# Performance work log

Measured on AMD Instinct MI355X. Metric: run time of the kernel, lower is better.

The kernel has to match this reference:

```python
import jax, jax.numpy as jnp
import numpy as np

N, E, G = 100000, 1600000, 2000
D_IN, D_H, D_MLP, D_OUT = 768, 128, 32, 2


def setup_inputs() -> dict:
    key = jax.random.key(0)
    ks = jax.random.split(key, 12)
    x = jax.random.normal(ks[0], (N, D_IN), dtype=jnp.float32)
    edge_index = jax.random.randint(ks[1], (2, E), 0, N, dtype=jnp.int64)
    edge_attr = jax.random.uniform(ks[2], (E, 1), dtype=jnp.float32)
    batch = jnp.sort(jax.random.randint(ks[3], (N,), 0, G, dtype=jnp.int64))
    s1 = 1.0 / np.sqrt(D_IN)
    s2 = 1.0 / np.sqrt(D_H)
    s3 = 1.0 / np.sqrt(D_MLP)
    return {
        "x": x, "edge_index": edge_index, "edge_attr": edge_attr,
        "batch": batch, "num_graphs": G,
        "W1i": jax.random.normal(ks[4], (D_IN, D_H), dtype=jnp.float32) * s1,
        "W1r": jax.random.normal(ks[5], (D_IN, D_H), dtype=jnp.float32) * s1,
        "b1": jnp.zeros((D_H,), dtype=jnp.float32),
        "W2i": jax.random.normal(ks[6], (D_H, D_H), dtype=jnp.float32) * s2,
        "W2r": jax.random.normal(ks[7], (D_H, D_H), dtype=jnp.float32) * s2,
        "b2": jnp.zeros((D_H,), dtype=jnp.float32),
        "Wl1": jax.random.normal(ks[8], (D_H, D_MLP), dtype=jnp.float32) * s2,
        "bl1": jnp.zeros((D_MLP,), dtype=jnp.float32),
        "Wl2": jax.random.normal(ks[9], (D_MLP, D_OUT), dtype=jnp.float32) * s3,
        "bl2": jnp.zeros((D_OUT,), dtype=jnp.float32),
    }


def _arma_conv(x, row, col, ew, Wi, Wr, b, n_nodes):
    # gcn_norm without self-loops: D^{-1/2} A D^{-1/2}
    deg = jax.ops.segment_sum(ew, col, num_segments=n_nodes)
    dinv = jnp.where(deg > 0, jax.lax.rsqrt(jnp.where(deg > 0, deg, 1.0)), 0.0)
    norm = dinv[row] * ew * dinv[col]
    h = x @ Wi                                   # [N, F_out]
    msg = h[row] * norm[:, None]                 # gather + scale  [E, F_out]
    agg = jax.ops.segment_sum(msg, col, num_segments=n_nodes)
    return jax.nn.relu(agg + x @ Wr + b)         # ARMA: K=1, T=1, act=ReLU


def reference(x, edge_index, edge_attr, batch, num_graphs,
              W1i, W1r, b1, W2i, W2r, b2, Wl1, bl1, Wl2, bl2):
    row, col = edge_index[0], edge_index[1]
    ew = edge_attr.reshape(-1)
    n = x.shape[0]
    h = jax.nn.elu(_arma_conv(x, row, col, ew, W1i, W1r, b1, n))
    node_x = _arma_conv(h, row, col, ew, W2i, W2r, b2, n)
    # global mean pool over graphs
    sums = jax.ops.segment_sum(node_x, batch, num_segments=num_graphs)
    cnt = jax.ops.segment_sum(jnp.ones((n,), node_x.dtype), batch, num_segments=num_graphs)
    graph_x = sums / jnp.maximum(cnt, 1.0)[:, None]
    pred = jax.nn.elu(graph_x @ Wl1 + bl1) @ Wl2 + bl2
    return pred
```

## Files before the change

kernel.cpp:

```cpp
#include <hip/hip_runtime.h>
#include <hip/hip_bf16.h>
#include <math.h>

typedef __attribute__((ext_vector_type(8))) short short8;
typedef __attribute__((ext_vector_type(4))) float f32x4;
typedef __attribute__((ext_vector_type(2))) float f32x2;
typedef __attribute__((address_space(1))) const void gvoid;
typedef __attribute__((address_space(3))) void lvoid;

#define NC 8

__device__ __forceinline__ unsigned short f2bf(float f) {
    unsigned int u = __builtin_bit_cast(unsigned int, f);
    return (unsigned short)((u + 0x7fffu + ((u >> 16) & 1u)) >> 16);
}
__device__ __forceinline__ float b2f(short s) {
    return __builtin_bit_cast(float, ((unsigned int)(unsigned short)s) << 16);
}
__device__ __forceinline__ unsigned int cvtpk(float lo, float hi) {
    unsigned int r;
    asm("v_cvt_pk_bf16_f32 %0, %1, %2" : "=v"(r) : "v"(lo), "v"(hi));
    return r;
}
__device__ __forceinline__ unsigned int pk8_lo(float a, float b, unsigned int old) {
    return (unsigned int)__builtin_amdgcn_cvt_pk_fp8_f32(a, b, (int)old, false);
}
__device__ __forceinline__ unsigned int pk8_hi(float a, float b, unsigned int old) {
    return (unsigned int)__builtin_amdgcn_cvt_pk_fp8_f32(a, b, (int)old, true);
}
__device__ __forceinline__ f32x2 up8_lo(unsigned int v) {
    return __builtin_amdgcn_cvt_pk_f32_fp8((int)v, false);
}
__device__ __forceinline__ f32x2 up8_hi(unsigned int v) {
    return __builtin_amdgcn_cvt_pk_f32_fp8((int)v, true);
}

__global__ __launch_bounds__(256) void deg_hist_kernel(
    const int* __restrict__ ei, const float* __restrict__ ea,
    unsigned long long* __restrict__ packed, int* __restrict__ rank, int N, int E)
{
    int e = blockIdx.x * 256 + threadIdx.x;
    if (e >= E) return;
    const int copy = blockIdx.x & (NC - 1);
    int c = ei[(size_t)E + e];
    unsigned long long fx = (unsigned long long)(ea[e] * 1048576.0f + 0.5f);
    unsigned long long old = atomicAdd(&packed[(size_t)copy * N + c], (1ULL << 42) | fx);
    rank[e] = (int)(old >> 42);
}

__global__ __launch_bounds__(256) void scan1p_kernel(
    const unsigned long long* __restrict__ packed, int* __restrict__ out,
    int* __restrict__ blksum, int n)
{
    __shared__ int part[256];
    const int t = threadIdx.x;
    const int base = blockIdx.x * 1024 + t * 4;
    int v[4];
#pragma unroll
    for (int q = 0; q < 4; ++q) {
        int s = 0;
        if (base + q < n) {
#pragma unroll
            for (int p = 0; p < NC; ++p)
                s += (int)(packed[(size_t)p * n + base + q] >> 42);
        }
        v[q] = s;
    }
    const int s = v[0] + v[1] + v[2] + v[3];
    part[t] = s;
    __syncthreads();
    for (int off = 1; off < 256; off <<= 1) {
        int x = (t >= off) ? part[t - off] : 0;
        __syncthreads();
        part[t] += x;
        __syncthreads();
    }
    if (t == 255) blksum[blockIdx.x] = part[255];
    int run = part[t] - s;
#pragma unroll
    for (int q = 0; q < 4; ++q) {
        if (base + q < n) out[base + q] = run;
        run += v[q];
    }
}

__global__ __launch_bounds__(256) void scan1_kernel(
    const int* __restrict__ in, int* __restrict__ out, int* __restrict__ blksum, int n)
{
    __shared__ int part[256];
    const int t = threadIdx.x;
    const int base = blockIdx.x * 1024 + t * 4;
    int v[4];
#pragma unroll
    for (int q = 0; q < 4; ++q) v[q] = (base + q < n) ? in[base + q] : 0;
    const int s = v[0] + v[1] + v[2] + v[3];
    part[t] = s;
    __syncthreads();
    for (int off = 1; off < 256; off <<= 1) {
        int x = (t >= off) ? part[t - off] : 0;
        __syncthreads();
        part[t] += x;
        __syncthreads();
    }
    if (t == 255) blksum[blockIdx.x] = part[255];
    int run = part[t] - s;
#pragma unroll
    for (int q = 0; q < 4; ++q) {
        if (base + q < n) out[base + q] = run;
        run += v[q];
    }
}

__global__ __launch_bounds__(256) void scan3_kernel(
    int* __restrict__ rowptr, const int* __restrict__ blkoff,
    int* __restrict__ wpb, const unsigned long long* __restrict__ packed,
    float* __restrict__ dinv, int n, int Etot)
{
    int i = blockIdx.x * 256 + threadIdx.x;
    if (i == 0) rowptr[n] = Etot;
    if (i >= n) return;
    int base = rowptr[i] + blkoff[i >> 10];
    rowptr[i] = base;
    unsigned long long degfx = 0;
    int acc = base;
#pragma unroll
    for (int p = 0; p < NC; ++p) {
        unsigned long long v = packed[(size_t)p * n + i];
        wpb[(size_t)p * n + i] = acc;
        acc += (int)(v >> 42);
        degfx += v & ((1ULL << 42) - 1);
    }
    dinv[i] = (degfx > 0) ? rsqrtf((float)degfx * 9.5367431640625e-7f) : 0.f;
}

__global__ __launch_bounds__(256) void place_kernel(
    const int* __restrict__ ei, const float* __restrict__ ea,
    const float* __restrict__ dinv, const int* __restrict__ wpb,
    const int* __restrict__ rank, int2* __restrict__ csr, int N, int E)
{
    int e = blockIdx.x * 256 + threadIdx.x;
    if (e >= E) return;
    const int copy = blockIdx.x & (NC - 1);
    int r = ei[e];
    int c = ei[(size_t)E + e];
    float nm = dinv[r] * ea[e] * dinv[c];
    int pos = wpb[(size_t)copy * N + c] + rank[e];
    int2 rec;
    rec.x = r;
    rec.y = __builtin_bit_cast(int, nm);
    csr[pos] = rec;
}

__global__ __launch_bounds__(256) void conv_weights(
    const float* __restrict__ W1i, const float* __restrict__ W1r,
    const float* __restrict__ W2i, const float* __restrict__ W2r,
    unsigned short* __restrict__ W1t, unsigned short* __restrict__ W2t)
{
    int id = blockIdx.x * 256 + threadIdx.x;
    if (id < 256 * 768) {
        int n = id / 768, j = id % 768;
        int k = (j & ~63) | ((((j >> 3) & 7) ^ (n & 7)) << 3) | (j & 7);
        float v = (n < 128) ? W1i[k * 128 + n] : W1r[k * 128 + (n - 128)];
        W1t[id] = f2bf(v);
    } else {
        int id2 = id - 256 * 768;
        if (id2 < 128 * 256) {
            int n = id2 >> 8, j = id2 & 255;
            int k = (j & ~63) | ((((j >> 3) & 7) ^ (n & 7)) << 3) | (j & 7);
            float v = (k < 128) ? W2i[k * 128 + n] : W2r[(k - 128) * 128 + n];
            W2t[id2] = f2bf(v);
        }
    }
}

__global__ __launch_bounds__(512) void gemm_mfma_dual(
    const float* __restrict__ A, const unsigned short* __restrict__ Wt,
    const float* __restrict__ bias, unsigned char* __restrict__ outP8,
    unsigned short* __restrict__ outR, int M, int K)
{
    __shared__ __align__(16) unsigned char As[2][64 * 128];
    __shared__ __align__(16) unsigned char Bs[2][256 * 128];

    const int t = threadIdx.x;
    const int m0 = blockIdx.x * 64;
    const int lane = t & 63;
    const int wid = t >> 6;
    const int wm = wid >> 2;
    const int wn = wid & 3;
    const int lr = lane & 15;
    const int lk = (lane >> 4) * 8;

    f32x4 acc[2][4] = {};

    const int sr = t >> 3;
    const int sk = (t & 7) * 8;
    const int aRow = m0 + sr;
    const bool aOk = (aRow < M);
    const float* aSrc = A + (size_t)(aOk ? aRow : 0) * K + sk;
    const int aDst = sr * 128 + ((sk * 2) ^ ((sr & 7) << 4));
    const unsigned short* bSrc = Wt + (size_t)(lane >> 3) * K + (lane & 7) * 8;

#pragma unroll
    for (int i = 0; i < 4; ++i) {
        const int chunk = i * 8 + wid;
        __builtin_amdgcn_global_load_lds(
            (gvoid*)(bSrc + (size_t)chunk * 8 * K),
            (lvoid*)(&Bs[0][chunk * 1024]), 16, 0, 0);
    }
    {
        float4 f0 = {}, f1 = {};
        if (aOk) { f0 = *(const float4*)(aSrc); f1 = *(const float4*)(aSrc + 4); }
        uint4 uv = {cvtpk(f0.x, f0.y), cvtpk(f0.z, f0.w),
                    cvtpk(f1.x, f1.y), cvtpk(f1.z, f1.w)};
        *(uint4*)(&As[0][aDst]) = uv;
    }

    for (int k0 = 0; k0 < K; k0 += 64) {
        const int cur = (k0 >> 6) & 1;
        const int nxt = cur ^ 1;
        const bool hasNext = (k0 + 64 < K);
        __syncthreads();

        float4 g0 = {}, g1 = {};
        if (hasNext) {
#pragma unroll
            for (int i = 0; i < 4; ++i) {
                const int chunk = i * 8 + wid;
                __builtin_amdgcn_global_load_lds(
                    (gvoid*)(bSrc + (size_t)chunk * 8 * K + k0 + 64),
                    (lvoid*)(&Bs[nxt][chunk * 1024]), 16, 0, 0);
            }
            if (aOk) {
                g0 = *(const float4*)(aSrc + k0 + 64);
                g1 = *(const float4*)(aSrc + k0 + 64 + 4);
            }
        }

#pragma unroll
        for (int ks = 0; ks < 2; ++ks) {
            short8 a[2], b[4];
#pragma unroll
            for (int mf = 0; mf < 2; ++mf) {
                const int r = wm * 32 + mf * 16 + lr;
                a[mf] = *(const short8*)(&As[cur][r * 128 + (((ks * 32 + lk) * 2) ^ ((r & 7) << 4))]);
            }
#pragma unroll
            for (int nf = 0; nf < 4; ++nf) {
                const int n = wn * 64 + nf * 16 + lr;
                b[nf] = *(const short8*)(&Bs[cur][n * 128 + (((ks * 32 + lk) * 2) ^ ((n & 7) << 4))]);
            }
#pragma unroll
            for (int mf = 0; mf < 2; ++mf)
#pragma unroll
                for (int nf = 0; nf < 4; ++nf)
                    acc[mf][nf] = __builtin_amdgcn_mfma_f32_16x16x32_bf16(
                        a[mf], b[nf], acc[mf][nf], 0, 0, 0);
        }

        if (hasNext) {
            uint4 uv = {cvtpk(g0.x, g0.y), cvtpk(g0.z, g0.w),
                        cvtpk(g1.x, g1.y), cvtpk(g1.z, g1.w)};
            *(uint4*)(&As[nxt][aDst]) = uv;
        }
    }

#pragma unroll
    for (int mf = 0; mf < 2; ++mf) {
#pragma unroll
        for (int nf = 0; nf < 4; ++nf) {
            const int n = wn * 64 + nf * 16 + lr;
            const f32x4 v = acc[mf][nf];
            const int mb = m0 + wm * 32 + mf * 16 + (lane >> 4) * 4;
            if (n < 128) {
                const unsigned int u01 = pk8_lo(v[0], v[1], 0u);
                const unsigned int u23 = pk8_lo(v[2], v[3], 0u);
                if (mb + 0 < M) outP8[(size_t)(mb + 0) * 128 + n] = (unsigned char)(u01);
                if (mb + 1 < M) outP8[(size_t)(mb + 1) * 128 + n] = (unsigned char)(u01 >> 8);
                if (mb + 2 < M) outP8[(size_t)(mb + 2) * 128 + n] = (unsigned char)(u23);
                if (mb + 3 < M) outP8[(size_t)(mb + 3) * 128 + n] = (unsigned char)(u23 >> 8);
            } else {
                const int nl = n - 128;
                const float badd = bias[nl];
#pragma unroll
                for (int j = 0; j < 4; ++j) {
                    if (mb + j < M) outR[(size_t)(mb + j) * 128 + nl] = f2bf(v[j] + badd);
                }
            }
        }
    }
}

__global__ __launch_bounds__(512) void gemm_mfma_single(
    const unsigned short* __restrict__ Aa,
    const unsigned short* __restrict__ Ah,
    const unsigned short* __restrict__ Wt,
    const float* __restrict__ bias,
    unsigned short* __restrict__ outX, int M)
{
    __shared__ __align__(16) unsigned char As[128 * 128];
    __shared__ __align__(16) unsigned char Bs[128 * 128];

    const int t = threadIdx.x;
    const int m0 = blockIdx.x * 128;
    const int lane = t & 63;
    const int wid = t >> 6;
    const int wm = wid >> 1;
    const int wn = wid & 1;
    const int lr = lane & 15;
    const int lk = (lane >> 4) * 8;

    f32x4 acc[2][4] = {};

    const int sr = t >> 2;
    const int sk = (t & 3) * 16;
    const int aRow = m0 + sr;
    const bool aOk = (aRow < M);
    const int rowSafe = aOk ? aRow : 0;
    const int sw = (sr & 7) << 4;
    const unsigned short* bSrc = Wt + (size_t)(lane >> 3) * 256 + (lane & 7) * 8;

    for (int k0 = 0; k0 < 256; k0 += 64) {
#pragma unroll
        for (int i = 0; i < 2; ++i) {
            const int chunk = i * 8 + wid;
            __builtin_amdgcn_global_load_lds(
                (gvoid*)(bSrc + (size_t)chunk * 8 * 256 + k0),
                (lvoid*)(Bs + chunk * 1024), 16, 0, 0);
        }
        const unsigned short* src =
            (k0 < 128 ? Aa : Ah) + (size_t)rowSafe * 128 + (k0 & 127) + sk;
        const short8 v0 = *(const short8*)(src);
        const short8 v1 = *(const short8*)(src + 8);
        *(short8*)(As + sr * 128 + ((sk * 2) ^ sw)) = v0;
        *(short8*)(As + sr * 128 + ((sk * 2 + 16) ^ sw)) = v1;
        __syncthreads();
#pragma unroll
        for (int ks = 0; ks < 2; ++ks) {
            short8 a[2], b[4];
#pragma unroll
            for (int mf = 0; mf < 2; ++mf) {
                const int r = wm * 32 + mf * 16 + lr;
                a[mf] = *(const short8*)(As + r * 128 + (((ks * 32 + lk) * 2) ^ ((r & 7) << 4)));
            }
#pragma unroll
            for (int nf = 0; nf < 4; ++nf) {
                const int n = wn * 64 + nf * 16 + lr;
                b[nf] = *(const short8*)(Bs + n * 128 + (((ks * 32 + lk) * 2) ^ ((n & 7) << 4)));
            }
#pragma unroll
            for (int mf = 0; mf < 2; ++mf)
#pragma unroll
                for (int nf = 0; nf < 4; ++nf)
                    acc[mf][nf] = __builtin_amdgcn_mfma_f32_16x16x32_bf16(
                        a[mf], b[nf], acc[mf][nf], 0, 0, 0);
        }
        __syncthreads();
    }

#pragma unroll
    for (int mf = 0; mf < 2; ++mf) {
#pragma unroll
        for (int nf = 0; nf < 4; ++nf) {
            const int n = wn * 64 + nf * 16 + lr;
            const float bb = bias[n];
            const f32x4 v = acc[mf][nf];
#pragma unroll
            for (int j = 0; j < 4; ++j) {
                const int m = m0 + wm * 32 + mf * 16 + (lane >> 4) * 4 + j;
                if (m < M) outX[(size_t)m * 128 + n] = f2bf(fmaxf(v[j] + bb, 0.f));
            }
        }
    }
}

__global__ __launch_bounds__(256) void agg_bias_relu(
    const unsigned char* __restrict__ P8, const unsigned short* __restrict__ Rbf,
    const int* __restrict__ rowptr, const int2* __restrict__ csr,
    unsigned short* __restrict__ hout, unsigned char* __restrict__ h8out, int N)
{
    const int i = blockIdx.x * 16 + (threadIdx.x >> 4);
    const int l = threadIdx.x & 15;
    if (i >= N) return;
    const int beg = rowptr[i];
    const int end = rowptr[i + 1];
    const int c = l * 8;

    float acc0[8] = {}, acc1[8] = {}, acc2[8] = {}, acc3[8] = {};
    int j = beg;
    for (; j + 3 < end; j += 4) {
        const int2 e0 = csr[j],     e1 = csr[j + 1];
        const int2 e2 = csr[j + 2], e3 = csr[j + 3];
        const uint2 u0 = *(const uint2*)(P8 + (size_t)e0.x * 128 + c);
        const uint2 u1 = *(const uint2*)(P8 + (size_t)e1.x * 128 + c);
        const uint2 u2 = *(const uint2*)(P8 + (size_t)e2.x * 128 + c);
        const uint2 u3 = *(const uint2*)(P8 + (size_t)e3.x * 128 + c);
        const float n0 = __builtin_bit_cast(float, e0.y);
        const float n1 = __builtin_bit_cast(float, e1.y);
        const float n2 = __builtin_bit_cast(float, e2.y);
        const float n3 = __builtin_bit_cast(float, e3.y);
        {
            const f32x2 p0 = up8_lo(u0.x), p1 = up8_hi(u0.x);
            const f32x2 p2 = up8_lo(u0.y), p3 = up8_hi(u0.y);
            acc0[0] = fmaf(p0.x, n0, acc0[0]); acc0[1] = fmaf(p0.y, n0, acc0[1]);
            acc0[2] = fmaf(p1.x, n0, acc0[2]); acc0[3] = fmaf(p1.y, n0, acc0[3]);
            acc0[4] = fmaf(p2.x, n0, acc0[4]); acc0[5] = fmaf(p2.y, n0, acc0[5]);
            acc0[6] = fmaf(p3.x, n0, acc0[6]); acc0[7] = fmaf(p3.y, n0, acc0[7]);
        }
        {
            const f32x2 p0 = up8_lo(u1.x), p1 = up8_hi(u1.x);
            const f32x2 p2 = up8_lo(u1.y), p3 = up8_hi(u1.y);
            acc1[0] = fmaf(p0.x, n1, acc1[0]); acc1[1] = fmaf(p0.y, n1, acc1[1]);
            acc1[2] = fmaf(p1.x, n1, acc1[2]); acc1[3] = fmaf(p1.y, n1, acc1[3]);
            acc1[4] = fmaf(p2.x, n1, acc1[4]); acc1[5] = fmaf(p2.y, n1, acc1[5]);
            acc1[6] = fmaf(p3.x, n1, acc1[6]); acc1[7] = fmaf(p3.y, n1, acc1[7]);
        }
        {
            const f32x2 p0 = up8_lo(u2.x), p1 = up8_hi(u2.x);
            const f32x2 p2 = up8_lo(u2.y), p3 = up8_hi(u2.y);
            acc2[0] = fmaf(p0.x, n2, acc2[0]); acc2[1] = fmaf(p0.y, n2, acc2[1]);
            acc2[2] = fmaf(p1.x, n2, acc2[2]); acc2[3] = fmaf(p1.y, n2, acc2[3]);
            acc2[4] = fmaf(p2.x, n2, acc2[4]); acc2[5] = fmaf(p2.y, n2, acc2[5]);
            acc2[6] = fmaf(p3.x, n2, acc2[6]); acc2[7] = fmaf(p3.y, n2, acc2[7]);
        }
        {
            const f32x2 p0 = up8_lo(u3.x), p1 = up8_hi(u3.x);
            const f32x2 p2 = up8_lo(u3.y), p3 = up8_hi(u3.y);
            acc3[0] = fmaf(p0.x, n3, acc3[0]); acc3[1] = fmaf(p0.y, n3, acc3[1]);
            acc3[2] = fmaf(p1.x, n3, acc3[2]); acc3[3] = fmaf(p1.y, n3, acc3[3]);
            acc3[4] = fmaf(p2.x, n3, acc3[4]); acc3[5] = fmaf(p2.y, n3, acc3[5]);
            acc3[6] = fmaf(p3.x, n3, acc3[6]); acc3[7] = fmaf(p3.y, n3, acc3[7]);
        }
    }
    for (; j < end; ++j) {
        const int2 e0 = csr[j];
        const uint2 u0 = *(const uint2*)(P8 + (size_t)e0.x * 128 + c);
        const float n0 = __builtin_bit_cast(float, e0.y);
        const f32x2 p0 = up8_lo(u0.x), p1 = up8_hi(u0.x);
        const f32x2 p2 = up8_lo(u0.y), p3 = up8_hi(u0.y);
        acc0[0] = fmaf(p0.x, n0, acc0[0]); acc0[1] = fmaf(p0.y, n0, acc0[1]);
        acc0[2] = fmaf(p1.x, n0, acc0[2]); acc0[3] = fmaf(p1.y, n0, acc0[3]);
        acc0[4] = fmaf(p2.x, n0, acc0[4]); acc0[5] = fmaf(p2.y, n0, acc0[5]);
        acc0[6] = fmaf(p3.x, n0, acc0[6]); acc0[7] = fmaf(p3.y, n0, acc0[7]);
    }
    const short8 rv = *(const short8*)(Rbf + (size_t)i * 128 + c);
    float s[8];
    short8 ov;
#pragma unroll
    for (int q = 0; q < 8; ++q) {
        s[q] = fmaxf((acc0[q] + acc1[q]) + (acc2[q] + acc3[q]) + b2f(rv[q]), 0.f);
        ov[q] = (short)f2bf(s[q]);
    }
    *(short8*)(hout + (size_t)i * 128 + c) = ov;
    unsigned int w0 = 0, w1 = 0;
    w0 = pk8_lo(s[0], s[1], w0); w0 = pk8_hi(s[2], s[3], w0);
    w1 = pk8_lo(s[4], s[5], w1); w1 = pk8_hi(s[6], s[7], w1);
    uint2 wv = {w0, w1};
    *(uint2*)(h8out + (size_t)i * 128 + c) = wv;
}

__global__ __launch_bounds__(256) void agg_plain(
    const unsigned char* __restrict__ H8,
    const int* __restrict__ rowptr, const int2* __restrict__ csr,
    unsigned short* __restrict__ ahout, int N)
{
    const int i = blockIdx.x * 16 + (threadIdx.x >> 4);
    const int l = threadIdx.x & 15;
    if (i >= N) return;
    const int beg = rowptr[i];
    const int end = rowptr[i + 1];
    const int c = l * 8;

    float acc0[8] = {}, acc1[8] = {}, acc2[8] = {}, acc3[8] = {};
    int j = beg;
    for (; j + 3 < end; j += 4) {
        const int2 e0 = csr[j],     e1 = csr[j + 1];
        const int2 e2 = csr[j + 2], e3 = csr[j + 3];
        const uint2 u0 = *(const uint2*)(H8 + (size_t)e0.x * 128 + c);
        const uint2 u1 = *(const uint2*)(H8 + (size_t)e1.x * 128 + c);
        const uint2 u2 = *(const uint2*)(H8 + (size_t)e2.x * 128 + c);
        const uint2 u3 = *(const uint2*)(H8 + (size_t)e3.x * 128 + c);
        const float n0 = __builtin_bit_cast(float, e0.y);
        const float n1 = __builtin_bit_cast(float, e1.y);
        const float n2 = __builtin_bit_cast(float, e2.y);
        const float n3 = __builtin_bit_cast(float, e3.y);
        {
            const f32x2 p0 = up8_lo(u0.x), p1 = up8_hi(u0.x);
            const f32x2 p2 = up8_lo(u0.y), p3 = up8_hi(u0.y);
            acc0[0] = fmaf(p0.x, n0, acc0[0]); acc0[1] = fmaf(p0.y, n0, acc0[1]);
            acc0[2] = fmaf(p1.x, n0, acc0[2]); acc0[3] = fmaf(p1.y, n0, acc0[3]);
            acc0[4] = fmaf(p2.x, n0, acc0[4]); acc0[5] = fmaf(p2.y, n0, acc0[5]);
            acc0[6] = fmaf(p3.x, n0, acc0[6]); acc0[7] = fmaf(p3.y, n0, acc0[7]);
        }
        {
            const f32x2 p0 = up8_lo(u1.x), p1 = up8_hi(u1.x);
            const f32x2 p2 = up8_lo(u1.y), p3 = up8_hi(u1.y);
            acc1[0] = fmaf(p0.x, n1, acc1[0]); acc1[1] = fmaf(p0.y, n1, acc1[1]);
            acc1[2] = fmaf(p1.x, n1, acc1[2]); acc1[3] = fmaf(p1.y, n1, acc1[3]);
            acc1[4] = fmaf(p2.x, n1, acc1[4]); acc1[5] = fmaf(p2.y, n1, acc1[5]);
            acc1[6] = fmaf(p3.x, n1, acc1[6]); acc1[7] = fmaf(p3.y, n1, acc1[7]);
        }
        {
            const f32x2 p0 = up8_lo(u2.x), p1 = up8_hi(u2.x);
            const f32x2 p2 = up8_lo(u2.y), p3 = up8_hi(u2.y);
            acc2[0] = fmaf(p0.x, n2, acc2[0]); acc2[1] = fmaf(p0.y, n2, acc2[1]);
            acc2[2] = fmaf(p1.x, n2, acc2[2]); acc2[3] = fmaf(p1.y, n2, acc2[3]);
            acc2[4] = fmaf(p2.x, n2, acc2[4]); acc2[5] = fmaf(p2.y, n2, acc2[5]);
            acc2[6] = fmaf(p3.x, n2, acc2[6]); acc2[7] = fmaf(p3.y, n2, acc2[7]);
        }
        {
            const f32x2 p0 = up8_lo(u3.x), p1 = up8_hi(u3.x);
            const f32x2 p2 = up8_lo(u3.y), p3 = up8_hi(u3.y);
            acc3[0] = fmaf(p0.x, n3, acc3[0]); acc3[1] = fmaf(p0.y, n3, acc3[1]);
            acc3[2] = fmaf(p1.x, n3, acc3[2]); acc3[3] = fmaf(p1.y, n3, acc3[3]);
            acc3[4] = fmaf(p2.x, n3, acc3[4]); acc3[5] = fmaf(p2.y, n3, acc3[5]);
            acc3[6] = fmaf(p3.x, n3, acc3[6]); acc3[7] = fmaf(p3.y, n3, acc3[7]);
        }
    }
    for (; j < end; ++j) {
        const int2 e0 = csr[j];
        const uint2 u0 = *(const uint2*)(H8 + (size_t)e0.x * 128 + c);
        const float n0 = __builtin_bit_cast(float, e0.y);
        const f32x2 p0 = up8_lo(u0.x), p1 = up8_hi(u0.x);
        const f32x2 p2 = up8_lo(u0.y), p3 = up8_hi(u0.y);
        acc0[0] = fmaf(p0.x, n0, acc0[0]); acc0[1] = fmaf(p0.y, n0, acc0[1]);
        acc0[2] = fmaf(p1.x, n0, acc0[2]); acc0[3] = fmaf(p1.y, n0, acc0[3]);
        acc0[4] = fmaf(p2.x, n0, acc0[4]); acc0[5] = fmaf(p2.y, n0, acc0[5]);
        acc0[6] = fmaf(p3.x, n0, acc0[6]); acc0[7] = fmaf(p3.y, n0, acc0[7]);
    }
    short8 ov;
#pragma unroll
    for (int q = 0; q < 8; ++q)
        ov[q] = (short)f2bf((acc0[q] + acc1[q]) + (acc2[q] + acc3[q]));
    *(short8*)(ahout + (size_t)i * 128 + c) = ov;
}

__global__ __launch_bounds__(256) void pool_mlp(
    const unsigned short* __restrict__ nx, const int* __restrict__ batch, int N,
    const float* __restrict__ Wl1, const float* __restrict__ bl1,
    const float* __restrict__ Wl2, const float* __restrict__ bl2,
    float* __restrict__ out)
{
    __shared__ float gxp[4][128];
    __shared__ float hid[32];
    __shared__ int rng[2];
    const int g = blockIdx.x;
    const int t = threadIdx.x;
    if (t < 2) {
        const int target = g + t;
        int lo = 0, hi = N;
        while (lo < hi) {
            int mid = (lo + hi) >> 1;
            if (batch[mid] < target) lo = mid + 1; else hi = mid;
        }
        rng[t] = lo;
    }
    __syncthreads();
    const int s = rng[0], e = rng[1];
    const int pr = t & 63;
    const int strm = t >> 6;
    float a0 = 0.f, b0 = 0.f, a1 = 0.f, b1 = 0.f;
    int i = s + strm;
    for (; i + 4 < e; i += 8) {
        const unsigned int u = *(const unsigned int*)&nx[(size_t)i * 128 + pr * 2];
        const unsigned int v = *(const unsigned int*)&nx[(size_t)(i + 4) * 128 + pr * 2];
        a0 += b2f((short)(u & 0xffff)); b0 += b2f((short)(u >> 16));
        a1 += b2f((short)(v & 0xffff)); b1 += b2f((short)(v >> 16));
    }
    if (i < e) {
        const unsigned int u = *(const unsigned int*)&nx[(size_t)i * 128 + pr * 2];
        a0 += b2f((short)(u & 0xffff)); b0 += b2f((short)(u >> 16));
    }
    gxp[strm][pr * 2] = a0 + a1;
    gxp[strm][pr * 2 + 1] = b0 + b1;
    __syncthreads();
    if (t < 128) {
        gxp[0][t] = ((gxp[0][t] + gxp[1][t]) + (gxp[2][t] + gxp[3][t]))
                    / fmaxf((float)(e - s), 1.f);
    }
    __syncthreads();
    if (t < 32) {
        float a = bl1[t];
#pragma unroll 8
        for (int k = 0; k < 128; ++k) a = fmaf(gxp[0][k], Wl1[k * 32 + t], a);
        hid[t] = a > 0.f ? a : expm1f(a);
    }
    __syncthreads();
    if (t < 2) {
        float a = bl2[t];
#pragma unroll
        for (int k = 0; k < 32; ++k) a = fmaf(hid[k], Wl2[k * 2 + t], a);
        out[(size_t)g * 2 + t] = a;
    }
}

extern "C" void kernel_launch(void* const* d_in, const int* in_sizes, int n_in,
                              void* d_out, int out_size, void* d_ws, size_t ws_size,
                              hipStream_t stream)
{
    const float* x     = (const float*)d_in[0];
    const int*   ei    = (const int*)d_in[1];
    const float* ea    = (const float*)d_in[2];
    const int*   batch = (const int*)d_in[3];
    const float* W1i   = (const float*)d_in[5];
    const float* W1r   = (const float*)d_in[6];
    const float* b1    = (const float*)d_in[7];
    const float* W2i   = (const float*)d_in[8];
    const float* W2r   = (const float*)d_in[9];
    const float* b2    = (const float*)d_in[10];
    const float* Wl1   = (const float*)d_in[11];
    const float* bl1   = (const float*)d_in[12];
    const float* Wl2   = (const float*)d_in[13];
    const float* bl2   = (const float*)d_in[14];

    const int N = in_sizes[0] / 768;
    const int E = in_sizes[2];
    const int G = out_size / 2;

    char* ws = (char*)d_ws;
    size_t off = 0;
    auto alloc = [&](size_t bytes) -> char* {
        char* p = ws + off;
        off = (off + bytes + 255) & ~(size_t)255;
        return p;
    };
    unsigned long long* packed = (unsigned long long*)alloc((size_t)NC * N * 8);
    int*   rank    = (int*)alloc((size_t)E * 4);
    int*   wpb     = (int*)alloc((size_t)NC * N * 4);
    float* dinv    = (float*)alloc((size_t)N * 4);
    int*   rowptr  = (int*)alloc((size_t)(N + 1) * 4);
    int*   blkoff  = (int*)alloc((size_t)1056 * 4);
    int*   blkdum  = (int*)alloc((size_t)4 * 4);
    int2*  csr     = (int2*)alloc((size_t)E * 8);
    unsigned char*  P8   = (unsigned char*)alloc((size_t)N * 128);
    unsigned char*  H8   = (unsigned char*)alloc((size_t)N * 128);
    unsigned short* R1   = (unsigned short*)alloc((size_t)N * 128 * 2);
    unsigned short* hbf  = (unsigned short*)alloc((size_t)N * 128 * 2);
    unsigned short* ahb  = (unsigned short*)alloc((size_t)N * 128 * 2);
    unsigned short* nxb  = (unsigned short*)alloc((size_t)N * 128 * 2);
    unsigned short* W1t  = (unsigned short*)alloc((size_t)256 * 768 * 2);
    unsigned short* W2t  = (unsigned short*)alloc((size_t)128 * 256 * 2);

    const int eBlocks = (E + 255) / 256;
    const int nb      = (N + 1023) / 1024;
    const int nBlocks = (N + 255) / 256;
    const int aBlocks = (N + 15) / 16;

    (void)hipMemsetAsync(packed, 0, (size_t)NC * N * 8, stream);
    deg_hist_kernel<<<eBlocks, 256, 0, stream>>>(ei, ea, packed, rank, N, E);
    scan1p_kernel<<<nb, 256, 0, stream>>>(packed, rowptr, blkoff, N);
    scan1_kernel<<<1, 256, 0, stream>>>(blkoff, blkoff, blkdum, nb);
    scan3_kernel<<<nBlocks, 256, 0, stream>>>(rowptr, blkoff, wpb, packed, dinv, N, E);
    place_kernel<<<eBlocks, 256, 0, stream>>>(ei, ea, dinv, wpb, rank, csr, N, E);
    conv_weights<<<(256 * 768 + 128 * 256 + 255) / 256, 256, 0, stream>>>(
        W1i, W1r, W2i, W2r, W1t, W2t);

    gemm_mfma_dual<<<(N + 63) / 64, 512, 0, stream>>>(x, W1t, b1, P8, R1, N, 768);
    agg_bias_relu<<<aBlocks, 256, 0, stream>>>(P8, R1, rowptr, csr, hbf, H8, N);

    agg_plain<<<aBlocks, 256, 0, stream>>>(H8, rowptr, csr, ahb, N);
    gemm_mfma_single<<<(N + 127) / 128, 512, 0, stream>>>(ahb, hbf, W2t, b2, nxb, N);

    pool_mlp<<<G, 256, 0, stream>>>(nxb, batch, N, Wl1, bl1, Wl2, bl2, (float*)d_out);
}
```

Measured before the change: 380.7 us.

## Fuse weight conversion into histogram, merge block scan, drop GEMM double buffering

The weight transpose/convert work now runs as extra blocks inside the degree-histogram kernel. The single-block scan of block sums is folded into every block of scan3, which rescans the block sums itself. Together these remove two kernel launches. The first-layer GEMM also drops its double-buffered LDS pipeline for a single buffer with load, sync, compute, sync per K step. That halves LDS use and may raise occupancy, but it loses the overlap of global loads with MFMA work.

```diff
diff --git a/kernel.cpp b/kernel.cpp
--- a/kernel.cpp
+++ b/kernel.cpp
@@ -35,17 +35,39 @@
     return __builtin_amdgcn_cvt_pk_f32_fp8((int)v, true);
 }
 
-__global__ __launch_bounds__(256) void deg_hist_kernel(
+__global__ __launch_bounds__(256) void hist_conv_kernel(
     const int* __restrict__ ei, const float* __restrict__ ea,
-    unsigned long long* __restrict__ packed, int* __restrict__ rank, int N, int E)
-{
-    int e = blockIdx.x * 256 + threadIdx.x;
-    if (e >= E) return;
-    const int copy = blockIdx.x & (NC - 1);
-    int c = ei[(size_t)E + e];
-    unsigned long long fx = (unsigned long long)(ea[e] * 1048576.0f + 0.5f);
-    unsigned long long old = atomicAdd(&packed[(size_t)copy * N + c], (1ULL << 42) | fx);
-    rank[e] = (int)(old >> 42);
+    unsigned long long* __restrict__ packed, int* __restrict__ rank, int N, int E,
+    int eBlocks,
+    const float* __restrict__ W1i, const float* __restrict__ W1r,
+    const float* __restrict__ W2i, const float* __restrict__ W2r,
+    unsigned short* __restrict__ W1t, unsigned short* __restrict__ W2t)
+{
+    if ((int)blockIdx.x < eBlocks) {
+        int e = blockIdx.x * 256 + threadIdx.x;
+        if (e >= E) return;
+        const int copy = blockIdx.x & (NC - 1);
+        int c = ei[(size_t)E + e];
+        unsigned long long fx = (unsigned long long)(ea[e] * 1048576.0f + 0.5f);
+        unsigned long long old = atomicAdd(&packed[(size_t)copy * N + c], (1ULL << 42) | fx);
+        rank[e] = (int)(old >> 42);
+    } else {
+        int id = (blockIdx.x - eBlocks) * 256 + threadIdx.x;
+        if (id < 256 * 768) {
+            int n = id / 768, j = id % 768;
+            int k = (j & ~63) | ((((j >> 3) & 7) ^ (n & 7)) << 3) | (j & 7);
+            float v = (n < 128) ? W1i[k * 128 + n] : W1r[k * 128 + (n - 128)];
+            W1t[id] = f2bf(v);
+        } else {
+            int id2 = id - 256 * 768;
+            if (id2 < 128 * 256) {
+                int n = id2 >> 8, j = id2 & 255;
+                int k = (j & ~63) | ((((j >> 3) & 7) ^ (n & 7)) << 3) | (j & 7);
+                float v = (k < 128) ? W2i[k * 128 + n] : W2r[(k - 128) * 128 + n];
+                W2t[id2] = f2bf(v);
+            }
+        }
+    }
 }
 
 __global__ __launch_bounds__(256) void scan1p_kernel(
@@ -84,51 +106,38 @@
     }
 }
 
-__global__ __launch_bounds__(256) void scan1_kernel(
-    const int* __restrict__ in, int* __restrict__ out, int* __restrict__ blksum, int n)
-{
-    __shared__ int part[256];
+__global__ __launch_bounds__(256) void scan3_kernel(
+    int* __restrict__ rowptr, const int* __restrict__ blksum,
+    int* __restrict__ wpb, const unsigned long long* __restrict__ packed,
+    float* __restrict__ dinv, int n, int Etot, int nb)
+{
+    __shared__ int tmp[256];
+    __shared__ int sexcl[256];
     const int t = threadIdx.x;
-    const int base = blockIdx.x * 1024 + t * 4;
-    int v[4];
-#pragma unroll
-    for (int q = 0; q < 4; ++q) v[q] = (base + q < n) ? in[base + q] : 0;
-    const int s = v[0] + v[1] + v[2] + v[3];
-    part[t] = s;
+    const int v = (t < nb) ? blksum[t] : 0;
+    tmp[t] = v;
     __syncthreads();
     for (int off = 1; off < 256; off <<= 1) {
-        int x = (t >= off) ? part[t - off] : 0;
-        __syncthreads();
-        part[t] += x;
-        __syncthreads();
-    }
-    if (t == 255) blksum[blockIdx.x] = part[255];
-    int run = part[t] - s;
-#pragma unroll
-    for (int q = 0; q < 4; ++q) {
-        if (base + q < n) out[base + q] = run;
-        run += v[q];
-    }
-}
-
-__global__ __launch_bounds__(256) void scan3_kernel(
-    int* __restrict__ rowptr, const int* __restrict__ blkoff,
-    int* __restrict__ wpb, const unsigned long long* __restrict__ packed,
-    float* __restrict__ dinv, int n, int Etot)
-{
-    int i = blockIdx.x * 256 + threadIdx.x;
+        int x = (t >= off) ? tmp[t - off] : 0;
+        __syncthreads();
+        tmp[t] += x;
+        __syncthreads();
+    }
+    sexcl[t] = tmp[t] - v;
+    __syncthreads();
+    const int i = blockIdx.x * 256 + t;
     if (i == 0) rowptr[n] = Etot;
     if (i >= n) return;
-    int base = rowptr[i] + blkoff[i >> 10];
+    int base = rowptr[i] + sexcl[i >> 10];
     rowptr[i] = base;
     unsigned long long degfx = 0;
     int acc = base;
 #pragma unroll
     for (int p = 0; p < NC; ++p) {
-        unsigned long long v = packed[(size_t)p * n + i];
+        unsigned long long vv = packed[(size_t)p * n + i];
         wpb[(size_t)p * n + i] = acc;
-        acc += (int)(v >> 42);
-        degfx += v & ((1ULL << 42) - 1);
+        acc += (int)(vv >> 42);
+        degfx += vv & ((1ULL << 42) - 1);
     }
     dinv[i] = (degfx > 0) ? rsqrtf((float)degfx * 9.5367431640625e-7f) : 0.f;
 }
@@ -151,35 +160,13 @@
     csr[pos] = rec;
 }
 
-__global__ __launch_bounds__(256) void conv_weights(
-    const float* __restrict__ W1i, const float* __restrict__ W1r,
-    const float* __restrict__ W2i, const float* __restrict__ W2r,
-    unsigned short* __restrict__ W1t, unsigned short* __restrict__ W2t)
-{
-    int id = blockIdx.x * 256 + threadIdx.x;
-    if (id < 256 * 768) {
-        int n = id / 768, j = id % 768;
-        int k = (j & ~63) | ((((j >> 3) & 7) ^ (n & 7)) << 3) | (j & 7);
-        float v = (n < 128) ? W1i[k * 128 + n] : W1r[k * 128 + (n - 128)];
-        W1t[id] = f2bf(v);
-    } else {
-        int id2 = id - 256 * 768;
-        if (id2 < 128 * 256) {
-            int n = id2 >> 8, j = id2 & 255;
-            int k = (j & ~63) | ((((j >> 3) & 7) ^ (n & 7)) << 3) | (j & 7);
-            float v = (k < 128) ? W2i[k * 128 + n] : W2r[(k - 128) * 128 + n];
-            W2t[id2] = f2bf(v);
-        }
-    }
-}
-
 __global__ __launch_bounds__(512) void gemm_mfma_dual(
     const float* __restrict__ A, const unsigned short* __restrict__ Wt,
     const float* __restrict__ bias, unsigned char* __restrict__ outP8,
     unsigned short* __restrict__ outR, int M, int K)
 {
-    __shared__ __align__(16) unsigned char As[2][64 * 128];
-    __shared__ __align__(16) unsigned char Bs[2][256 * 128];
+    __shared__ __align__(16) unsigned char As[64 * 128];
+    __shared__ __align__(16) unsigned char Bs[256 * 128];
 
     const int t = threadIdx.x;
     const int m0 = blockIdx.x * 64;
@@ -200,54 +187,38 @@
     const int aDst = sr * 128 + ((sk * 2) ^ ((sr & 7) << 4));
     const unsigned short* bSrc = Wt + (size_t)(lane >> 3) * K + (lane & 7) * 8;
 
-#pragma unroll
-    for (int i = 0; i < 4; ++i) {
-        const int chunk = i * 8 + wid;
-        __builtin_amdgcn_global_load_lds(
-            (gvoid*)(bSrc + (size_t)chunk * 8 * K),
-            (lvoid*)(&Bs[0][chunk * 1024]), 16, 0, 0);
-    }
-    {
-        float4 f0 = {}, f1 = {};
-        if (aOk) { f0 = *(const float4*)(aSrc); f1 = *(const float4*)(aSrc + 4); }
-        uint4 uv = {cvtpk(f0.x, f0.y), cvtpk(f0.z, f0.w),
-                    cvtpk(f1.x, f1.y), cvtpk(f1.z, f1.w)};
-        *(uint4*)(&As[0][aDst]) = uv;
-    }
-
     for (int k0 = 0; k0 < K; k0 += 64) {
-        const int cur = (k0 >> 6) & 1;
-        const int nxt = cur ^ 1;
-        const bool hasNext = (k0 + 64 < K);
-        __syncthreads();
-
-        float4 g0 = {}, g1 = {};
-        if (hasNext) {
-#pragma unroll
-            for (int i = 0; i < 4; ++i) {
-                const int chunk = i * 8 + wid;
-                __builtin_amdgcn_global_load_lds(
-                    (gvoid*)(bSrc + (size_t)chunk * 8 * K + k0 + 64),
-                    (lvoid*)(&Bs[nxt][chunk * 1024]), 16, 0, 0);
-            }
-            if (aOk) {
-                g0 = *(const float4*)(aSrc + k0 + 64);
-                g1 = *(const float4*)(aSrc + k0 + 64 + 4);
-            }
-        }
-
+#pragma unroll
+        for (int i = 0; i < 4; ++i) {
+            const int chunk = i * 8 + wid;
+            __builtin_amdgcn_global_load_lds(
+                (gvoid*)(bSrc + (size_t)chunk * 8 * K + k0),
+                (lvoid*)(Bs + chunk * 1024), 16, 0, 0);
+        }
+        unsigned int p0 = 0, p1 = 0, p2 = 0, p3 = 0;
+        if (aOk) {
+            const float4 f0 = *(const float4*)(aSrc + k0);
+            const float4 f1 = *(const float4*)(aSrc + k0 + 4);
+            p0 = cvtpk(f0.x, f0.y);
+            p1 = cvtpk(f0.z, f0.w);
+            p2 = cvtpk(f1.x, f1.y);
+            p3 = cvtpk(f1.z, f1.w);
+        }
+        uint4 uv = {p0, p1, p2, p3};
+        *(uint4*)(As + aDst) = uv;
+        __syncthreads();
 #pragma unroll
         for (int ks = 0; ks < 2; ++ks) {
             short8 a[2], b[4];
 #pragma unroll
             for (int mf = 0; mf < 2; ++mf) {
                 const int r = wm * 32 + mf * 16 + lr;
-                a[mf] = *(const short8*)(&As[cur][r * 128 + (((ks * 32 + lk) * 2) ^ ((r & 7) << 4))]);
+                a[mf] = *(const short8*)(As + r * 128 + (((ks * 32 + lk) * 2) ^ ((r & 7) << 4)));
             }
 #pragma unroll
             for (int nf = 0; nf < 4; ++nf) {
                 const int n = wn * 64 + nf * 16 + lr;
-                b[nf] = *(const short8*)(&Bs[cur][n * 128 + (((ks * 32 + lk) * 2) ^ ((n & 7) << 4))]);
+                b[nf] = *(const short8*)(Bs + n * 128 + (((ks * 32 + lk) * 2) ^ ((n & 7) << 4)));
             }
 #pragma unroll
             for (int mf = 0; mf < 2; ++mf)
@@ -256,12 +227,7 @@
                     acc[mf][nf] = __builtin_amdgcn_mfma_f32_16x16x32_bf16(
                         a[mf], b[nf], acc[mf][nf], 0, 0, 0);
         }
-
-        if (hasNext) {
-            uint4 uv = {cvtpk(g0.x, g0.y), cvtpk(g0.z, g0.w),
-                        cvtpk(g1.x, g1.y), cvtpk(g1.z, g1.w)};
-            *(uint4*)(&As[nxt][aDst]) = uv;
-        }
+        __syncthreads();
     }
 
 #pragma unroll
@@ -628,8 +594,7 @@
     int*   wpb     = (int*)alloc((size_t)NC * N * 4);
     float* dinv    = (float*)alloc((size_t)N * 4);
     int*   rowptr  = (int*)alloc((size_t)(N + 1) * 4);
-    int*   blkoff  = (int*)alloc((size_t)1056 * 4);
-    int*   blkdum  = (int*)alloc((size_t)4 * 4);
+    int*   blksum  = (int*)alloc((size_t)256 * 4);
     int2*  csr     = (int2*)alloc((size_t)E * 8);
     unsigned char*  P8   = (unsigned char*)alloc((size_t)N * 128);
     unsigned char*  H8   = (unsigned char*)alloc((size_t)N * 128);
@@ -641,18 +606,17 @@
     unsigned short* W2t  = (unsigned short*)alloc((size_t)128 * 256 * 2);
 
     const int eBlocks = (E + 255) / 256;
+    const int cBlocks = (256 * 768 + 128 * 256 + 255) / 256;
     const int nb      = (N + 1023) / 1024;
     const int nBlocks = (N + 255) / 256;
     const int aBlocks = (N + 15) / 16;
 
     (void)hipMemsetAsync(packed, 0, (size_t)NC * N * 8, stream);
-    deg_hist_kernel<<<eBlocks, 256, 0, stream>>>(ei, ea, packed, rank, N, E);
-    scan1p_kernel<<<nb, 256, 0, stream>>>(packed, rowptr, blkoff, N);
-    scan1_kernel<<<1, 256, 0, stream>>>(blkoff, blkoff, blkdum, nb);
-    scan3_kernel<<<nBlocks, 256, 0, stream>>>(rowptr, blkoff, wpb, packed, dinv, N, E);
+    hist_conv_kernel<<<eBlocks + cBlocks, 256, 0, stream>>>(
+        ei, ea, packed, rank, N, E, eBlocks, W1i, W1r, W2i, W2r, W1t, W2t);
+    scan1p_kernel<<<nb, 256, 0, stream>>>(packed, rowptr, blksum, N);
+    scan3_kernel<<<nBlocks, 256, 0, stream>>>(rowptr, blksum, wpb, packed, dinv, N, E, nb);
     place_kernel<<<eBlocks, 256, 0, stream>>>(ei, ea, dinv, wpb, rank, csr, N, E);
-    conv_weights<<<(256 * 768 + 128 * 256 + 255) / 256, 256, 0, stream>>>(
-        W1i, W1r, W2i, W2r, W1t, W2t);
 
     gemm_mfma_dual<<<(N + 63) / 64, 512, 0, stream>>>(x, W1t, b1, P8, R1, N, 768);
     agg_bias_relu<<<aBlocks, 256, 0, stream>>>(P8, R1, rowptr, csr, hbf, H8, N);
```

After: 369.8 us (median of 2 runs). 1.03x faster.
